# Optimization experiments

Measured on AMD Instinct MI355X. Metric: run time of the kernel, lower is better.

Reference implementation:

```python
import jax, jax.numpy as jnp
import numpy as np

RADIUS = 0.2
K_SAMPLES = 32
SPATIAL_STRIDE = 2
TEMPORAL_K = 3
BN_EPS = 1e-5


def setup_inputs() -> dict:
    key = jax.random.key(0)
    ks = jax.random.split(key, 5)
    B, L, N, C = 4, 8, 2048, 32
    mid, out = 64, 128
    xyzs = jax.random.uniform(ks[0], (B, L, N, 3), dtype=jnp.float32)
    features = jax.random.normal(ks[1], (B, L, C, N), dtype=jnp.float32)
    conv_d_w = jax.random.normal(ks[2], (mid, 3), dtype=jnp.float32) * 0.3
    conv_f_w = jax.random.normal(ks[3], (mid, C), dtype=jnp.float32) * 0.1
    bn_gamma = jnp.ones((TEMPORAL_K * mid,), jnp.float32)
    bn_beta = jnp.zeros((TEMPORAL_K * mid,), jnp.float32)
    temporal_w = jax.random.normal(ks[4], (out, TEMPORAL_K * mid), dtype=jnp.float32) * 0.05
    return {"xyzs": xyzs, "features": features, "conv_d_w": conv_d_w,
            "conv_f_w": conv_f_w, "bn_gamma": bn_gamma, "bn_beta": bn_beta,
            "temporal_w": temporal_w}


def _fps(xyz, m):
    # furthest point sampling: xyz (N,3) -> (m,) int32 indices, first index is 0
    n = xyz.shape[0]
    def body(carry, _):
        dists, last = carry
        d = jnp.sum((xyz - xyz[last]) ** 2, axis=-1)
        dists = jnp.minimum(dists, d)
        nxt = jnp.argmax(dists).astype(jnp.int32)
        return (dists, nxt), last
    init = (jnp.full((n,), jnp.finfo(xyz.dtype).max, xyz.dtype), jnp.array(0, jnp.int32))
    _, idx = jax.lax.scan(body, init, None, length=m)
    return idx


def _ball_query(anchor, neighbor):
    # anchor (M,3), neighbor (N,3) -> (M,K) int32; first K points within RADIUS,
    # missing slots filled with first valid index (0 if none), matching pointnet2.
    n = neighbor.shape[0]
    d2 = jnp.sum((anchor[:, None, :] - neighbor[None, :, :]) ** 2, axis=-1)  # (M,N)
    cand = jnp.where(d2 < RADIUS * RADIUS, jnp.arange(n, dtype=jnp.int32)[None, :], n)
    cand = jnp.sort(cand, axis=1)[:, :K_SAMPLES]  # first K in index order
    first = cand[:, 0]
    safe_first = jnp.where(first == n, 0, first)
    return jnp.where(cand == n, safe_first[:, None], cand)


def _group(pts, idx):
    # pts (BL, N, D), idx (BL, M, K) -> (BL, M, K, D)
    return jnp.take_along_axis(pts[:, None, :, :], idx[..., None], axis=2)


def _forward(xyzs, features, conv_d_w, conv_f_w, bn_gamma, bn_beta, temporal_w):
    B, L, N, _ = xyzs.shape
    C = features.shape[2]
    M = N // SPATIAL_STRIDE
    KM = bn_gamma.shape[0]  # TEMPORAL_K * mid

    # temporal zero padding [1,1]
    xp = jnp.concatenate([jnp.zeros((B, 1, N, 3), xyzs.dtype), xyzs,
                          jnp.zeros((B, 1, N, 3), xyzs.dtype)], axis=1)  # (B,L+2,N,3)
    fp = jnp.concatenate([jnp.zeros((B, 1, C, N), features.dtype), features,
                          jnp.zeros((B, 1, C, N), features.dtype)], axis=1)

    # anchors from each center frame t=1..L
    center = xp[:, 1:L + 1].reshape(B * L, N, 3)
    anchor_idx = jax.vmap(lambda x: _fps(x, M))(center)            # (BL, M)
    anchor = jnp.take_along_axis(center, anchor_idx[..., None], axis=1)  # (BL, M, 3)

    offset_feats = []
    for o in range(TEMPORAL_K):  # neighbor frames t-1, t, t+1
        nb = xp[:, o:o + L].reshape(B * L, N, 3)
        nf = jnp.swapaxes(fp[:, o:o + L].reshape(B * L, C, N), 1, 2)  # (BL,N,C)
        idx = jax.vmap(_ball_query)(anchor, nb)                      # (BL,M,K)
        g_xyz = _group(nb, idx)                                      # (BL,M,K,3)
        g_f = _group(nf, idx)                                        # (BL,M,K,C)
        disp = g_xyz - anchor[:, :, None, :]
        d_out = jnp.einsum('oc,bmkc->bmko', conv_d_w, disp)          # (BL,M,K,mid)
        f_out = jnp.einsum('oc,bmkc->bmko', conv_f_w, g_f)
        # multiplication aggregation + sum pooling over neighbors
        offset_feats.append(jnp.sum(f_out * d_out, axis=2))          # (BL,M,mid)

    x = jnp.concatenate(offset_feats, axis=-1)                       # (BL,M,KM)
    x = jnp.transpose(x.reshape(B, L, M, KM), (0, 1, 3, 2))          # (B,L,KM,M)

    # BatchNorm1d applied per frame (torch loop calls BN once per t): stats over (B, M)
    mean = jnp.mean(x, axis=(0, 3), keepdims=True)
    var = jnp.var(x, axis=(0, 3), keepdims=True)
    x = (x - mean) * jax.lax.rsqrt(var + BN_EPS)
    x = x * bn_gamma[None, None, :, None] + bn_beta[None, None, :, None]
    x = jax.nn.relu(x)

    new_features = jnp.einsum('ok,blkm->blom', temporal_w, x)        # (B,L,out,M)
    new_xyzs = anchor.reshape(B, L, M, 3)
    return new_xyzs, new_features


def reference(xyzs, features, conv_d_w, conv_f_w, bn_gamma, bn_beta, temporal_w):
    return _forward(xyzs, features, conv_d_w, conv_f_w, bn_gamma, bn_beta, temporal_w)
```

## Files before the change

kernel.cpp:

```cpp
#include <hip/hip_runtime.h>

#define NB_B 4
#define NB_L 8
#define NB_N 2048
#define NB_C 32
#define NB_M 1024

#define ANCH_OFF  0
#define FT_OFF    98304
#define XRAW_OFF  2195456
#define STATS_OFF 8486912

__global__ __launch_bounds__(256) void transpose_kernel(const float* __restrict__ f,
                                                        float* __restrict__ ft) {
  __shared__ float tile[NB_C][65];
  int frame = blockIdx.x >> 5;
  int n0 = (blockIdx.x & 31) * 64;
  int t = threadIdx.x;
  const float* src = f + (size_t)frame * NB_C * NB_N;
#pragma unroll
  for (int i = 0; i < 8; ++i) {
    int q = t + i * 256;
    int c = q >> 6, n = q & 63;
    tile[c][n] = src[c * NB_N + n0 + n];
  }
  __syncthreads();
  float* dst = ft + ((size_t)frame * NB_N + n0) * NB_C;
  int n = t >> 2, c0 = (t & 3) * 8;
  float v[8];
#pragma unroll
  for (int i = 0; i < 8; ++i) v[i] = tile[c0 + i][n];
  float4 w0 = {v[0], v[1], v[2], v[3]};
  float4 w1 = {v[4], v[5], v[6], v[7]};
  *(float4*)(dst + n * NB_C + c0) = w0;
  *(float4*)(dst + n * NB_C + c0 + 4) = w1;
}

__device__ __forceinline__ unsigned long long umax64(unsigned long long a,
                                                     unsigned long long b) {
  return a > b ? a : b;
}

template <int CTRL>
__device__ __forceinline__ unsigned long long dpp_xch64(unsigned long long v) {
  int lo = (int)(unsigned)v;
  int hi = (int)(unsigned)(v >> 32);
  int plo = __builtin_amdgcn_update_dpp(0, lo, CTRL, 0xF, 0xF, false);
  int phi = __builtin_amdgcn_update_dpp(0, hi, CTRL, 0xF, 0xF, false);
  return ((unsigned long long)(unsigned)phi << 32) | (unsigned)plo;
}

__device__ __forceinline__ unsigned long long swz_xor16_64(unsigned long long v) {
  int lo = (int)(unsigned)v;
  int hi = (int)(unsigned)(v >> 32);
  int plo = __builtin_amdgcn_ds_swizzle(lo, 0x401F);
  int phi = __builtin_amdgcn_ds_swizzle(hi, 0x401F);
  return ((unsigned long long)(unsigned)phi << 32) | (unsigned)plo;
}

#define DPP_XOR1 0xB1
#define DPP_XOR2 0x4E
#define DPP_HMIR 0x141
#define DPP_MIR  0x140

#define FPS_T 512

__global__ __launch_bounds__(FPS_T) void fps_kernel(const float* __restrict__ xyzs,
                                                    float* __restrict__ anchors,
                                                    float* __restrict__ d_out) {
  int cloud = blockIdx.x;
  int t = threadIdx.x;
  int lane = t & 63;
  const float* xyz = xyzs + (size_t)cloud * NB_N * 3;
  __shared__ float4 pos4[NB_N];
  __shared__ unsigned long long red[2][8];
  __shared__ int hist[NB_M];
  for (int i = t; i < NB_N; i += FPS_T) {
    float x = xyz[i * 3 + 0];
    float y = xyz[i * 3 + 1];
    float z = xyz[i * 3 + 2];
    pos4[i] = make_float4(x, y, z, 0.f);
  }
  __syncthreads();
  float px[4], py[4], pz[4], dist[4];
  unsigned inv[4];
#pragma unroll
  for (int j = 0; j < 4; ++j) {
    int n = j * FPS_T + t;
    float4 p = pos4[n];
    px[j] = p.x; py[j] = p.y; pz[j] = p.z;
    dist[j] = 3.402823466e38f;
    inv[j] = 0x7FFFFFFFu - (unsigned)n;
  }
  int last = 0;
  float4 sp = pos4[0];
  float lx = sp.x, ly = sp.y, lz = sp.z;
  for (int m = 0; m < NB_M; ++m) {
    if (t == 0) hist[m] = last;
    unsigned long long best = 0;
#pragma unroll
    for (int j = 0; j < 4; ++j) {
      float dx = __fsub_rn(px[j], lx);
      float dy = __fsub_rn(py[j], ly);
      float dz = __fsub_rn(pz[j], lz);
      float d = __fadd_rn(__fadd_rn(__fmul_rn(dx, dx), __fmul_rn(dy, dy)),
                          __fmul_rn(dz, dz));
      float dj = fminf(dist[j], d);
      dist[j] = dj;
      unsigned long long pk =
          ((unsigned long long)__float_as_uint(dj) << 32) | inv[j];
      best = umax64(best, pk);
    }
    best = umax64(best, dpp_xch64<DPP_XOR1>(best));
    best = umax64(best, dpp_xch64<DPP_XOR2>(best));
    best = umax64(best, dpp_xch64<DPP_HMIR>(best));
    best = umax64(best, dpp_xch64<DPP_MIR>(best));
    best = umax64(best, swz_xor16_64(best));
    best = umax64(best, __shfl_xor(best, 32));
    if (lane == 0) red[m & 1][t >> 6] = best;
    __syncthreads();
    unsigned long long g = red[m & 1][lane & 7];
    g = umax64(g, dpp_xch64<DPP_XOR1>(g));
    g = umax64(g, dpp_xch64<DPP_XOR2>(g));
    g = umax64(g, dpp_xch64<DPP_HMIR>(g));
    last = 0x7FFFFFFF - (int)(unsigned)g;
    float4 p = pos4[last];
    lx = p.x; ly = p.y; lz = p.z;
  }
  __syncthreads();
  for (int mm = t; mm < NB_M; mm += FPS_T) {
    int idx = hist[mm];
    float4 p = pos4[idx];
    size_t o = ((size_t)cloud * NB_M + mm) * 3;
    anchors[o + 0] = p.x; anchors[o + 1] = p.y; anchors[o + 2] = p.z;
    d_out[o + 0] = p.x;   d_out[o + 1] = p.y;   d_out[o + 2] = p.z;
  }
}

__device__ __forceinline__ float rdlane(float v, int l) {
  return __int_as_float(__builtin_amdgcn_readlane(__float_as_int(v), l));
}

__global__ __launch_bounds__(256) void bq_conv_kernel(
    const float* __restrict__ xyzs, const float* __restrict__ ft,
    const float* __restrict__ anchors, const float* __restrict__ conv_d_w,
    const float* __restrict__ conv_f_w, float* __restrict__ x_raw) {
  int w = threadIdx.x >> 6, lane = threadIdx.x & 63;
  int task = blockIdx.x * 4 + w;
  int cloud = task / 3072;
  int rem = task - cloud * 3072;
  int o = rem >> 10, m = rem & 1023;
  int b = cloud >> 3, l = cloud & 7;
  int nl = l + o - 1;
  float* xout = x_raw + (((size_t)(l * NB_B + b) * NB_M + m) * 192 + o * 64);
  __shared__ int list_s[4][32];
  if (nl < 0 || nl >= NB_L) {
    xout[lane] = 0.0f;
    return;
  }
  const float4* wf4 = (const float4*)(conv_f_w + lane * 32);
  float wf[32];
#pragma unroll
  for (int i = 0; i < 8; ++i) {
    float4 v = wf4[i];
    wf[i * 4 + 0] = v.x; wf[i * 4 + 1] = v.y;
    wf[i * 4 + 2] = v.z; wf[i * 4 + 3] = v.w;
  }
  float wd0 = conv_d_w[lane * 3 + 0];
  float wd1 = conv_d_w[lane * 3 + 1];
  float wd2 = conv_d_w[lane * 3 + 2];

  const float* ap = anchors + ((size_t)cloud * NB_M + m) * 3;
  float ax = ap[0], ay = ap[1], az = ap[2];
  const float* nb = xyzs + (size_t)(b * NB_L + nl) * NB_N * 3;

  unsigned long long lmlt = (1ull << lane) - 1ull;
  int count = 0;
  for (int it = 0; it < 16; ++it) {
    int n0 = it * 128 + lane;
    int n1 = n0 + 64;
    float x0 = nb[n0 * 3 + 0], y0 = nb[n0 * 3 + 1], z0 = nb[n0 * 3 + 2];
    float x1 = nb[n1 * 3 + 0], y1 = nb[n1 * 3 + 1], z1 = nb[n1 * 3 + 2];
    float dx0 = __fsub_rn(ax, x0), dy0 = __fsub_rn(ay, y0), dz0 = __fsub_rn(az, z0);
    float d20 = __fadd_rn(__fadd_rn(__fmul_rn(dx0, dx0), __fmul_rn(dy0, dy0)),
                          __fmul_rn(dz0, dz0));
    float dx1 = __fsub_rn(ax, x1), dy1 = __fsub_rn(ay, y1), dz1 = __fsub_rn(az, z1);
    float d21 = __fadd_rn(__fadd_rn(__fmul_rn(dx1, dx1), __fmul_rn(dy1, dy1)),
                          __fmul_rn(dz1, dz1));
    bool h0 = d20 < 0.04f;
    bool h1 = d21 < 0.04f;
    unsigned long long m0 = __ballot(h0);
    int p0 = count + __popcll(m0 & lmlt);
    if (h0 && p0 < 32) list_s[w][p0] = n0;
    int c0 = count + __popcll(m0);
    unsigned long long m1 = __ballot(h1);
    int p1 = c0 + __popcll(m1 & lmlt);
    if (h1 && p1 < 32) list_s[w][p1] = n1;
    count = c0 + __popcll(m1);
    if (count >= 32) break;
  }
  asm volatile("s_waitcnt lgkmcnt(0)" ::: "memory");
  int cnt = count < 32 ? count : 32;
  int first = (cnt > 0) ? list_s[w][0] : 0;

  int k = lane & 31;
  int idxk = (k < cnt) ? list_s[w][k] : first;
  float bx = nb[idxk * 3 + 0], by = nb[idxk * 3 + 1], bz = nb[idxk * 3 + 2];
  float d0 = __fsub_rn(bx, ax);
  float d1 = __fsub_rn(by, ay);
  float d2v = __fsub_rn(bz, az);

  int c = lane & 31;
  int kbase = (lane >> 5) << 4;
  const float* ftf = ft + (size_t)(b * NB_L + nl) * NB_N * NB_C + c;
  float G0 = 0.f, G1 = 0.f, G2 = 0.f;
#pragma unroll 4
  for (int i = 0; i < 16; ++i) {
    int kk = kbase + i;
    int ik = (kk < cnt) ? list_s[w][kk] : first;
    float fv = ftf[(size_t)ik * NB_C];
    float e0 = __shfl(d0, kk);
    float e1 = __shfl(d1, kk);
    float e2 = __shfl(d2v, kk);
    G0 = fmaf(fv, e0, G0);
    G1 = fmaf(fv, e1, G1);
    G2 = fmaf(fv, e2, G2);
  }
  G0 += __shfl_xor(G0, 32);
  G1 += __shfl_xor(G1, 32);
  G2 += __shfl_xor(G2, 32);

  float acc = 0.f;
#pragma unroll
  for (int cc = 0; cc < 32; ++cc) {
    float g0 = rdlane(G0, cc);
    float g1 = rdlane(G1, cc);
    float g2 = rdlane(G2, cc);
    float tt = fmaf(g2, wd2, fmaf(g1, wd1, g0 * wd0));
    acc = fmaf(wf[cc], tt, acc);
  }
  xout[lane] = acc;
}

__global__ __launch_bounds__(192) void bn_stats_kernel(const float* __restrict__ x_raw,
                                                       float* __restrict__ stats) {
  int bid = blockIdx.x;
  int mt = bid & 3, bb = (bid >> 2) & 3, l = bid >> 4;
  int c = threadIdx.x;
  const float* p = x_raw + ((size_t)(l * NB_B + bb) * NB_M + mt * 256) * 192 + c;
  float s = 0.f, s2 = 0.f;
  for (int i = 0; i < 256; ++i) {
    float v = p[(size_t)i * 192];
    s += v;
    s2 = fmaf(v, v, s2);
  }
  atomicAdd(&stats[l * 192 + c], s);
  atomicAdd(&stats[1536 + l * 192 + c], s2);
}

__global__ __launch_bounds__(256) void final_kernel(
    const float* __restrict__ x_raw, const float* __restrict__ stats,
    const float* __restrict__ gamma, const float* __restrict__ beta,
    const float* __restrict__ tw, float* __restrict__ out) {
  __shared__ __align__(16) float xn[32 * 192];
  __shared__ __align__(16) float wt[64 * 132];
  __shared__ float sc[192], sh[192];
  int cloud = blockIdx.x >> 5;
  int mt = blockIdx.x & 31;
  int b = cloud >> 3, l = cloud & 7;
  int m0 = mt * 32;
  int t = threadIdx.x;
  if (t < 192) {
    float mean = stats[l * 192 + t] * (1.0f / 4096.0f);
    float ex2 = stats[1536 + l * 192 + t] * (1.0f / 4096.0f);
    float var = fmaxf(ex2 - mean * mean, 0.0f);
    float g = gamma[t] / sqrtf(var + 1e-5f);
    sc[t] = g;
    sh[t] = fmaf(-mean, g, beta[t]);
  }
  __syncthreads();
  const float* xp = x_raw + ((size_t)(l * NB_B + b) * NB_M + m0) * 192;
#pragma unroll
  for (int i = 0; i < 24; ++i) {
    int q = t + i * 256;
    int cc = q % 192;
    float v = xp[q];
    xn[q] = fmaxf(fmaf(v, sc[cc], sh[cc]), 0.0f);
  }
  float acc[4][4];
#pragma unroll
  for (int i = 0; i < 4; ++i)
#pragma unroll
    for (int j = 0; j < 4; ++j) acc[i][j] = 0.f;
  int o0 = (t & 31) * 4;
  int mg = (t >> 5) * 4;
  for (int kt = 0; kt < 3; ++kt) {
    __syncthreads();
#pragma unroll
    for (int i = 0; i < 32; ++i) {
      int q = t + i * 256;
      int oo = q >> 6, kk = q & 63;
      wt[kk * 132 + oo] = tw[oo * 192 + kt * 64 + kk];
    }
    __syncthreads();
#pragma unroll
    for (int kk = 0; kk < 64; kk += 4) {
      float a[4][4], bb2[4][4];
#pragma unroll
      for (int mi = 0; mi < 4; ++mi) {
        float4 v = *(const float4*)&xn[(mg + mi) * 192 + kt * 64 + kk];
        a[mi][0] = v.x; a[mi][1] = v.y; a[mi][2] = v.z; a[mi][3] = v.w;
      }
#pragma unroll
      for (int j = 0; j < 4; ++j) {
        float4 v = *(const float4*)&wt[(kk + j) * 132 + o0];
        bb2[j][0] = v.x; bb2[j][1] = v.y; bb2[j][2] = v.z; bb2[j][3] = v.w;
      }
#pragma unroll
      for (int mi = 0; mi < 4; ++mi)
#pragma unroll
        for (int j = 0; j < 4; ++j)
#pragma unroll
          for (int oi = 0; oi < 4; ++oi)
            acc[mi][oi] = fmaf(a[mi][j], bb2[j][oi], acc[mi][oi]);
    }
  }
  float* op = out + 98304 + ((size_t)cloud * 128 + o0) * NB_M + m0 + mg;
#pragma unroll
  for (int oi = 0; oi < 4; ++oi) {
    float4 v = {acc[0][oi], acc[1][oi], acc[2][oi], acc[3][oi]};
    *(float4*)(op + (size_t)oi * NB_M) = v;
  }
}

extern "C" void kernel_launch(void* const* d_in, const int* in_sizes, int n_in,
                              void* d_out, int out_size, void* d_ws, size_t ws_size,
                              hipStream_t stream) {
  const float* xyzs = (const float*)d_in[0];
  const float* features = (const float*)d_in[1];
  const float* conv_d_w = (const float*)d_in[2];
  const float* conv_f_w = (const float*)d_in[3];
  const float* bn_gamma = (const float*)d_in[4];
  const float* bn_beta = (const float*)d_in[5];
  const float* temporal_w = (const float*)d_in[6];
  float* ws = (float*)d_ws;
  float* anchors = ws + ANCH_OFF;
  float* ft = ws + FT_OFF;
  float* xraw = ws + XRAW_OFF;
  float* stats = ws + STATS_OFF;
  float* out = (float*)d_out;

  hipMemsetAsync(stats, 0, 3072 * sizeof(float), stream);
  transpose_kernel<<<1024, 256, 0, stream>>>(features, ft);
  fps_kernel<<<32, FPS_T, 0, stream>>>(xyzs, anchors, out);
  bq_conv_kernel<<<24576, 256, 0, stream>>>(xyzs, ft, anchors, conv_d_w,
                                            conv_f_w, xraw);
  bn_stats_kernel<<<128, 192, 0, stream>>>(xraw, stats);
  final_kernel<<<1024, 256, 0, stream>>>(xraw, stats, bn_gamma, bn_beta,
                                         temporal_w, out);
}
```

Before: 864.7 us.

## Carry winner coordinates through FPS reduction and batch ball-query scans

In furthest point sampling, the wave reduction now uses permlane16/32 swap instructions in place of ds_swizzle and a shuffle. The winning point's coordinates travel with the argmax key through shared memory and the final DPP steps, so the dependent LDS lookup of pos4[last] on the serial critical path goes away. The ball query now evaluates 512 points per batch with eight ballots before compacting, trading a coarser early exit for more memory-level parallelism. The argmax reduction now moves extra registers, and batching may load more points than needed when neighbours are found early.

```diff
diff --git a/kernel.cpp b/kernel.cpp
--- a/kernel.cpp
+++ b/kernel.cpp
@@ -50,18 +50,48 @@
   return ((unsigned long long)(unsigned)phi << 32) | (unsigned)plo;
 }
 
-__device__ __forceinline__ unsigned long long swz_xor16_64(unsigned long long v) {
-  int lo = (int)(unsigned)v;
-  int hi = (int)(unsigned)(v >> 32);
-  int plo = __builtin_amdgcn_ds_swizzle(lo, 0x401F);
-  int phi = __builtin_amdgcn_ds_swizzle(hi, 0x401F);
-  return ((unsigned long long)(unsigned)phi << 32) | (unsigned)plo;
+__device__ __forceinline__ unsigned long long plane16_max(unsigned long long v) {
+  int alo = (int)(unsigned)v, blo = alo;
+  int ahi = (int)(unsigned)(v >> 32), bhi = ahi;
+  asm("v_permlane16_swap_b32 %0, %1" : "+v"(alo), "+v"(blo));
+  asm("v_permlane16_swap_b32 %0, %1" : "+v"(ahi), "+v"(bhi));
+  unsigned long long A = ((unsigned long long)(unsigned)ahi << 32) | (unsigned)alo;
+  unsigned long long B = ((unsigned long long)(unsigned)bhi << 32) | (unsigned)blo;
+  return umax64(A, B);
+}
+
+__device__ __forceinline__ unsigned long long plane32_max(unsigned long long v) {
+  int alo = (int)(unsigned)v, blo = alo;
+  int ahi = (int)(unsigned)(v >> 32), bhi = ahi;
+  asm("v_permlane32_swap_b32 %0, %1" : "+v"(alo), "+v"(blo));
+  asm("v_permlane32_swap_b32 %0, %1" : "+v"(ahi), "+v"(bhi));
+  unsigned long long A = ((unsigned long long)(unsigned)ahi << 32) | (unsigned)alo;
+  unsigned long long B = ((unsigned long long)(unsigned)bhi << 32) | (unsigned)blo;
+  return umax64(A, B);
 }
 
 #define DPP_XOR1 0xB1
 #define DPP_XOR2 0x4E
 #define DPP_HMIR 0x141
 #define DPP_MIR  0x140
+
+template <int CTRL>
+__device__ __forceinline__ void argmax_step(unsigned long long& g, float& x,
+                                            float& y, float& z) {
+  int glo = (int)(unsigned)g;
+  int ghi = (int)(unsigned)(g >> 32);
+  int olo = __builtin_amdgcn_update_dpp(0, glo, CTRL, 0xF, 0xF, false);
+  int ohi = __builtin_amdgcn_update_dpp(0, ghi, CTRL, 0xF, 0xF, false);
+  int ox = __builtin_amdgcn_update_dpp(0, __float_as_int(x), CTRL, 0xF, 0xF, false);
+  int oy = __builtin_amdgcn_update_dpp(0, __float_as_int(y), CTRL, 0xF, 0xF, false);
+  int oz = __builtin_amdgcn_update_dpp(0, __float_as_int(z), CTRL, 0xF, 0xF, false);
+  unsigned long long og = ((unsigned long long)(unsigned)ohi << 32) | (unsigned)olo;
+  bool take = og > g;
+  g = take ? og : g;
+  x = take ? __int_as_float(ox) : x;
+  y = take ? __int_as_float(oy) : y;
+  z = take ? __int_as_float(oz) : z;
+}
 
 #define FPS_T 512
 
@@ -70,10 +100,12 @@
                                                     float* __restrict__ d_out) {
   int cloud = blockIdx.x;
   int t = threadIdx.x;
+  int w = t >> 6;
   int lane = t & 63;
   const float* xyz = xyzs + (size_t)cloud * NB_N * 3;
   __shared__ float4 pos4[NB_N];
-  __shared__ unsigned long long red[2][8];
+  __shared__ unsigned long long skey[2][8];
+  __shared__ float4 spos[2][8];
   __shared__ int hist[NB_M];
   for (int i = t; i < NB_N; i += FPS_T) {
     float x = xyz[i * 3 + 0];
@@ -97,6 +129,7 @@
   float lx = sp.x, ly = sp.y, lz = sp.z;
   for (int m = 0; m < NB_M; ++m) {
     if (t == 0) hist[m] = last;
+    unsigned long long pk[4];
     unsigned long long best = 0;
 #pragma unroll
     for (int j = 0; j < 4; ++j) {
@@ -107,25 +140,33 @@
                           __fmul_rn(dz, dz));
       float dj = fminf(dist[j], d);
       dist[j] = dj;
-      unsigned long long pk =
-          ((unsigned long long)__float_as_uint(dj) << 32) | inv[j];
-      best = umax64(best, pk);
+      pk[j] = ((unsigned long long)__float_as_uint(dj) << 32) | inv[j];
+      best = umax64(best, pk[j]);
     }
     best = umax64(best, dpp_xch64<DPP_XOR1>(best));
     best = umax64(best, dpp_xch64<DPP_XOR2>(best));
     best = umax64(best, dpp_xch64<DPP_HMIR>(best));
     best = umax64(best, dpp_xch64<DPP_MIR>(best));
-    best = umax64(best, swz_xor16_64(best));
-    best = umax64(best, __shfl_xor(best, 32));
-    if (lane == 0) red[m & 1][t >> 6] = best;
+    best = plane16_max(best);
+    best = plane32_max(best);
+    float sx = px[0], sy = py[0], sz = pz[0];
+    if (pk[1] == best) { sx = px[1]; sy = py[1]; sz = pz[1]; }
+    if (pk[2] == best) { sx = px[2]; sy = py[2]; sz = pz[2]; }
+    if (pk[3] == best) { sx = px[3]; sy = py[3]; sz = pz[3]; }
+    bool win = (pk[0] == best) | (pk[1] == best) | (pk[2] == best) | (pk[3] == best);
+    if (win) {
+      skey[m & 1][w] = best;
+      spos[m & 1][w] = make_float4(sx, sy, sz, 0.f);
+    }
     __syncthreads();
-    unsigned long long g = red[m & 1][lane & 7];
-    g = umax64(g, dpp_xch64<DPP_XOR1>(g));
-    g = umax64(g, dpp_xch64<DPP_XOR2>(g));
-    g = umax64(g, dpp_xch64<DPP_HMIR>(g));
+    unsigned long long g = skey[m & 1][lane & 7];
+    float4 s = spos[m & 1][lane & 7];
+    float gx = s.x, gy = s.y, gz = s.z;
+    argmax_step<DPP_XOR1>(g, gx, gy, gz);
+    argmax_step<DPP_XOR2>(g, gx, gy, gz);
+    argmax_step<DPP_HMIR>(g, gx, gy, gz);
     last = 0x7FFFFFFF - (int)(unsigned)g;
-    float4 p = pos4[last];
-    lx = p.x; ly = p.y; lz = p.z;
+    lx = gx; ly = gy; lz = gz;
   }
   __syncthreads();
   for (int mm = t; mm < NB_M; mm += FPS_T) {
@@ -176,27 +217,26 @@
 
   unsigned long long lmlt = (1ull << lane) - 1ull;
   int count = 0;
-  for (int it = 0; it < 16; ++it) {
-    int n0 = it * 128 + lane;
-    int n1 = n0 + 64;
-    float x0 = nb[n0 * 3 + 0], y0 = nb[n0 * 3 + 1], z0 = nb[n0 * 3 + 2];
-    float x1 = nb[n1 * 3 + 0], y1 = nb[n1 * 3 + 1], z1 = nb[n1 * 3 + 2];
-    float dx0 = __fsub_rn(ax, x0), dy0 = __fsub_rn(ay, y0), dz0 = __fsub_rn(az, z0);
-    float d20 = __fadd_rn(__fadd_rn(__fmul_rn(dx0, dx0), __fmul_rn(dy0, dy0)),
-                          __fmul_rn(dz0, dz0));
-    float dx1 = __fsub_rn(ax, x1), dy1 = __fsub_rn(ay, y1), dz1 = __fsub_rn(az, z1);
-    float d21 = __fadd_rn(__fadd_rn(__fmul_rn(dx1, dx1), __fmul_rn(dy1, dy1)),
-                          __fmul_rn(dz1, dz1));
-    bool h0 = d20 < 0.04f;
-    bool h1 = d21 < 0.04f;
-    unsigned long long m0 = __ballot(h0);
-    int p0 = count + __popcll(m0 & lmlt);
-    if (h0 && p0 < 32) list_s[w][p0] = n0;
-    int c0 = count + __popcll(m0);
-    unsigned long long m1 = __ballot(h1);
-    int p1 = c0 + __popcll(m1 & lmlt);
-    if (h1 && p1 < 32) list_s[w][p1] = n1;
-    count = c0 + __popcll(m1);
+  for (int batch = 0; batch < 4; ++batch) {
+    unsigned long long bm[8];
+#pragma unroll
+    for (int c2 = 0; c2 < 8; ++c2) {
+      int n = batch * 512 + c2 * 64 + lane;
+      float x = nb[n * 3 + 0], y = nb[n * 3 + 1], z = nb[n * 3 + 2];
+      float dx = __fsub_rn(ax, x);
+      float dy = __fsub_rn(ay, y);
+      float dz = __fsub_rn(az, z);
+      float d2 = __fadd_rn(__fadd_rn(__fmul_rn(dx, dx), __fmul_rn(dy, dy)),
+                           __fmul_rn(dz, dz));
+      bm[c2] = __ballot(d2 < 0.04f);
+    }
+#pragma unroll
+    for (int c2 = 0; c2 < 8; ++c2) {
+      bool hit = (bm[c2] >> lane) & 1;
+      int pos = count + __popcll(bm[c2] & lmlt);
+      if (hit && pos < 32) list_s[w][pos] = batch * 512 + c2 * 64 + lane;
+      count += __popcll(bm[c2]);
+    }
     if (count >= 32) break;
   }
   asm volatile("s_waitcnt lgkmcnt(0)" ::: "memory");
```

New measurement: 1.083 ms. 1.25x slower.

## Batch ball-query ballots, process four anchors per wave, shorten FPS reduction

Applied to the files above, without the earlier changes.

The FPS kernel stops its in-wave reduction at 16-lane groups and writes 32 partial maxima to shared memory. Each lane then reads two of them and finishes with DPP steps, removing the swizzle and cross-half shuffle. The ball-query/conv kernel now has each wave handle four consecutive anchors, loading the conv weights once per wave instead of once per anchor. Its neighbor scan issues eight ballots per batch before compacting, which exposes more memory-level parallelism. The cost is a coarser early exit (512 points per batch) and a grid four times smaller, which may lower occupancy and latency hiding.

```diff
diff --git a/kernel.cpp b/kernel.cpp
--- a/kernel.cpp
+++ b/kernel.cpp
@@ -50,14 +50,6 @@
   return ((unsigned long long)(unsigned)phi << 32) | (unsigned)plo;
 }
 
-__device__ __forceinline__ unsigned long long swz_xor16_64(unsigned long long v) {
-  int lo = (int)(unsigned)v;
-  int hi = (int)(unsigned)(v >> 32);
-  int plo = __builtin_amdgcn_ds_swizzle(lo, 0x401F);
-  int phi = __builtin_amdgcn_ds_swizzle(hi, 0x401F);
-  return ((unsigned long long)(unsigned)phi << 32) | (unsigned)plo;
-}
-
 #define DPP_XOR1 0xB1
 #define DPP_XOR2 0x4E
 #define DPP_HMIR 0x141
@@ -70,10 +62,11 @@
                                                     float* __restrict__ d_out) {
   int cloud = blockIdx.x;
   int t = threadIdx.x;
+  int w = t >> 6;
   int lane = t & 63;
   const float* xyz = xyzs + (size_t)cloud * NB_N * 3;
   __shared__ float4 pos4[NB_N];
-  __shared__ unsigned long long red[2][8];
+  __shared__ __align__(16) unsigned long long slots32[2][32];
   __shared__ int hist[NB_M];
   for (int i = t; i < NB_N; i += FPS_T) {
     float x = xyz[i * 3 + 0];
@@ -95,8 +88,11 @@
   int last = 0;
   float4 sp = pos4[0];
   float lx = sp.x, ly = sp.y, lz = sp.z;
+  int sidx = w * 4 + (lane >> 4);
+  bool swrite = (lane & 15) == 0;
   for (int m = 0; m < NB_M; ++m) {
     if (t == 0) hist[m] = last;
+    int par = m & 1;
     unsigned long long best = 0;
 #pragma unroll
     for (int j = 0; j < 4; ++j) {
@@ -115,14 +111,14 @@
     best = umax64(best, dpp_xch64<DPP_XOR2>(best));
     best = umax64(best, dpp_xch64<DPP_HMIR>(best));
     best = umax64(best, dpp_xch64<DPP_MIR>(best));
-    best = umax64(best, swz_xor16_64(best));
-    best = umax64(best, __shfl_xor(best, 32));
-    if (lane == 0) red[m & 1][t >> 6] = best;
+    if (swrite) slots32[par][sidx] = best;
     __syncthreads();
-    unsigned long long g = red[m & 1][lane & 7];
+    ulonglong2 pr2 = *(const ulonglong2*)&slots32[par][(lane & 15) * 2];
+    unsigned long long g = umax64(pr2.x, pr2.y);
     g = umax64(g, dpp_xch64<DPP_XOR1>(g));
     g = umax64(g, dpp_xch64<DPP_XOR2>(g));
     g = umax64(g, dpp_xch64<DPP_HMIR>(g));
+    g = umax64(g, dpp_xch64<DPP_MIR>(g));
     last = 0x7FFFFFFF - (int)(unsigned)g;
     float4 p = pos4[last];
     lx = p.x; ly = p.y; lz = p.z;
@@ -141,21 +137,26 @@
   return __int_as_float(__builtin_amdgcn_readlane(__float_as_int(v), l));
 }
 
+#define BQ_WAVES 4
+#define BQ_TPW 4
+
 __global__ __launch_bounds__(256) void bq_conv_kernel(
     const float* __restrict__ xyzs, const float* __restrict__ ft,
     const float* __restrict__ anchors, const float* __restrict__ conv_d_w,
     const float* __restrict__ conv_f_w, float* __restrict__ x_raw) {
   int w = threadIdx.x >> 6, lane = threadIdx.x & 63;
-  int task = blockIdx.x * 4 + w;
-  int cloud = task / 3072;
-  int rem = task - cloud * 3072;
-  int o = rem >> 10, m = rem & 1023;
+  int gw = blockIdx.x * BQ_WAVES + w;
+  int task0 = gw * BQ_TPW;
+  int cloud = task0 / 3072;
+  int rem = task0 - cloud * 3072;
+  int o = rem >> 10, m0 = rem & 1023;
   int b = cloud >> 3, l = cloud & 7;
   int nl = l + o - 1;
-  float* xout = x_raw + (((size_t)(l * NB_B + b) * NB_M + m) * 192 + o * 64);
-  __shared__ int list_s[4][32];
+  __shared__ int list_s[BQ_WAVES][32];
+  float* xbase = x_raw + ((size_t)(l * NB_B + b) * NB_M + m0) * 192 + o * 64;
   if (nl < 0 || nl >= NB_L) {
-    xout[lane] = 0.0f;
+#pragma unroll
+    for (int t4 = 0; t4 < BQ_TPW; ++t4) xbase[(size_t)t4 * 192 + lane] = 0.0f;
     return;
   }
   const float4* wf4 = (const float4*)(conv_f_w + lane * 32);
@@ -170,76 +171,78 @@
   float wd1 = conv_d_w[lane * 3 + 1];
   float wd2 = conv_d_w[lane * 3 + 2];
 
-  const float* ap = anchors + ((size_t)cloud * NB_M + m) * 3;
-  float ax = ap[0], ay = ap[1], az = ap[2];
   const float* nb = xyzs + (size_t)(b * NB_L + nl) * NB_N * 3;
-
+  const float* ftf = ft + (size_t)(b * NB_L + nl) * NB_N * NB_C + (lane & 31);
   unsigned long long lmlt = (1ull << lane) - 1ull;
-  int count = 0;
-  for (int it = 0; it < 16; ++it) {
-    int n0 = it * 128 + lane;
-    int n1 = n0 + 64;
-    float x0 = nb[n0 * 3 + 0], y0 = nb[n0 * 3 + 1], z0 = nb[n0 * 3 + 2];
-    float x1 = nb[n1 * 3 + 0], y1 = nb[n1 * 3 + 1], z1 = nb[n1 * 3 + 2];
-    float dx0 = __fsub_rn(ax, x0), dy0 = __fsub_rn(ay, y0), dz0 = __fsub_rn(az, z0);
-    float d20 = __fadd_rn(__fadd_rn(__fmul_rn(dx0, dx0), __fmul_rn(dy0, dy0)),
-                          __fmul_rn(dz0, dz0));
-    float dx1 = __fsub_rn(ax, x1), dy1 = __fsub_rn(ay, y1), dz1 = __fsub_rn(az, z1);
-    float d21 = __fadd_rn(__fadd_rn(__fmul_rn(dx1, dx1), __fmul_rn(dy1, dy1)),
-                          __fmul_rn(dz1, dz1));
-    bool h0 = d20 < 0.04f;
-    bool h1 = d21 < 0.04f;
-    unsigned long long m0 = __ballot(h0);
-    int p0 = count + __popcll(m0 & lmlt);
-    if (h0 && p0 < 32) list_s[w][p0] = n0;
-    int c0 = count + __popcll(m0);
-    unsigned long long m1 = __ballot(h1);
-    int p1 = c0 + __popcll(m1 & lmlt);
-    if (h1 && p1 < 32) list_s[w][p1] = n1;
-    count = c0 + __popcll(m1);
-    if (count >= 32) break;
-  }
-  asm volatile("s_waitcnt lgkmcnt(0)" ::: "memory");
-  int cnt = count < 32 ? count : 32;
-  int first = (cnt > 0) ? list_s[w][0] : 0;
-
-  int k = lane & 31;
-  int idxk = (k < cnt) ? list_s[w][k] : first;
-  float bx = nb[idxk * 3 + 0], by = nb[idxk * 3 + 1], bz = nb[idxk * 3 + 2];
-  float d0 = __fsub_rn(bx, ax);
-  float d1 = __fsub_rn(by, ay);
-  float d2v = __fsub_rn(bz, az);
-
-  int c = lane & 31;
   int kbase = (lane >> 5) << 4;
-  const float* ftf = ft + (size_t)(b * NB_L + nl) * NB_N * NB_C + c;
-  float G0 = 0.f, G1 = 0.f, G2 = 0.f;
-#pragma unroll 4
-  for (int i = 0; i < 16; ++i) {
-    int kk = kbase + i;
-    int ik = (kk < cnt) ? list_s[w][kk] : first;
-    float fv = ftf[(size_t)ik * NB_C];
-    float e0 = __shfl(d0, kk);
-    float e1 = __shfl(d1, kk);
-    float e2 = __shfl(d2v, kk);
-    G0 = fmaf(fv, e0, G0);
-    G1 = fmaf(fv, e1, G1);
-    G2 = fmaf(fv, e2, G2);
-  }
-  G0 += __shfl_xor(G0, 32);
-  G1 += __shfl_xor(G1, 32);
-  G2 += __shfl_xor(G2, 32);
-
-  float acc = 0.f;
-#pragma unroll
-  for (int cc = 0; cc < 32; ++cc) {
-    float g0 = rdlane(G0, cc);
-    float g1 = rdlane(G1, cc);
-    float g2 = rdlane(G2, cc);
-    float tt = fmaf(g2, wd2, fmaf(g1, wd1, g0 * wd0));
-    acc = fmaf(wf[cc], tt, acc);
-  }
-  xout[lane] = acc;
+
+  for (int t4 = 0; t4 < BQ_TPW; ++t4) {
+    int m = m0 + t4;
+    const float* ap = anchors + ((size_t)cloud * NB_M + m) * 3;
+    float ax = ap[0], ay = ap[1], az = ap[2];
+
+    int count = 0;
+    for (int batch = 0; batch < 4; ++batch) {
+      unsigned long long bm[8];
+#pragma unroll
+      for (int c2 = 0; c2 < 8; ++c2) {
+        int n = batch * 512 + c2 * 64 + lane;
+        float x = nb[n * 3 + 0], y = nb[n * 3 + 1], z = nb[n * 3 + 2];
+        float dx = __fsub_rn(ax, x);
+        float dy = __fsub_rn(ay, y);
+        float dz = __fsub_rn(az, z);
+        float d2 = __fadd_rn(__fadd_rn(__fmul_rn(dx, dx), __fmul_rn(dy, dy)),
+                             __fmul_rn(dz, dz));
+        bm[c2] = __ballot(d2 < 0.04f);
+      }
+#pragma unroll
+      for (int c2 = 0; c2 < 8; ++c2) {
+        bool hit = (bm[c2] >> lane) & 1;
+        int pos = count + __popcll(bm[c2] & lmlt);
+        if (hit && pos < 32) list_s[w][pos] = batch * 512 + c2 * 64 + lane;
+        count += __popcll(bm[c2]);
+      }
+      if (count >= 32) break;
+    }
+    asm volatile("s_waitcnt lgkmcnt(0)" ::: "memory");
+    int cnt = count < 32 ? count : 32;
+    int first = (cnt > 0) ? list_s[w][0] : 0;
+
+    int k = lane & 31;
+    int idxk = (k < cnt) ? list_s[w][k] : first;
+    float bx = nb[idxk * 3 + 0], by = nb[idxk * 3 + 1], bz = nb[idxk * 3 + 2];
+    float d0 = __fsub_rn(bx, ax);
+    float d1 = __fsub_rn(by, ay);
+    float d2v = __fsub_rn(bz, az);
+
+    float G0 = 0.f, G1 = 0.f, G2 = 0.f;
+#pragma unroll 8
+    for (int i = 0; i < 16; ++i) {
+      int kk = kbase + i;
+      int ik = (kk < cnt) ? list_s[w][kk] : first;
+      float fv = ftf[(size_t)ik * NB_C];
+      float e0 = __shfl(d0, kk);
+      float e1 = __shfl(d1, kk);
+      float e2 = __shfl(d2v, kk);
+      G0 = fmaf(fv, e0, G0);
+      G1 = fmaf(fv, e1, G1);
+      G2 = fmaf(fv, e2, G2);
+    }
+    G0 += __shfl_xor(G0, 32);
+    G1 += __shfl_xor(G1, 32);
+    G2 += __shfl_xor(G2, 32);
+
+    float acc = 0.f;
+#pragma unroll
+    for (int cc = 0; cc < 32; ++cc) {
+      float g0 = rdlane(G0, cc);
+      float g1 = rdlane(G1, cc);
+      float g2 = rdlane(G2, cc);
+      float tt = fmaf(g2, wd2, fmaf(g1, wd1, g0 * wd0));
+      acc = fmaf(wf[cc], tt, acc);
+    }
+    xbase[(size_t)t4 * 192 + lane] = acc;
+  }
 }
 
 __global__ __launch_bounds__(192) void bn_stats_kernel(const float* __restrict__ x_raw,
@@ -353,8 +356,8 @@
   hipMemsetAsync(stats, 0, 3072 * sizeof(float), stream);
   transpose_kernel<<<1024, 256, 0, stream>>>(features, ft);
   fps_kernel<<<32, FPS_T, 0, stream>>>(xyzs, anchors, out);
-  bq_conv_kernel<<<24576, 256, 0, stream>>>(xyzs, ft, anchors, conv_d_w,
-                                            conv_f_w, xraw);
+  bq_conv_kernel<<<6144, 256, 0, stream>>>(xyzs, ft, anchors, conv_d_w,
+                                           conv_f_w, xraw);
   bn_stats_kernel<<<128, 192, 0, stream>>>(xraw, stats);
   final_kernel<<<1024, 256, 0, stream>>>(xraw, stats, bn_gamma, bn_beta,
                                          temporal_w, out);
```

After: 770.9 us. -10.8%, faster.
